# Kernel tuning notes

Hardware: AMD Instinct MI355X
Metric: run time of the kernel (lower is better)

Reference implementation:

```python
import jax, jax.numpy as jnp
import numpy as np

M1 = M2 = M3 = 8  # truncated Hartley modes (min(modes, in_channels) in original)


def dht(x):
    # Discrete Hartley transform via 3D FFT over spatial axes: real - imag
    r = jnp.fft.fftn(x, axes=(2, 3, 4))
    return r.real - r.imag


def _mul(a, w):
    # 'bixyz,ioxyz->boxyz' mode-wise channel mixing
    return jnp.einsum('bixyz,ioxyz->boxyz', a, w)


def setup_inputs() -> dict:
    key = jax.random.key(0)
    ks = jax.random.split(key, 5)
    B, Ci, Co = 2, 64, 64
    S1 = S2 = S3 = 64
    scale = 1.0 / (Ci * Co)
    x = jax.random.normal(ks[0], (B, Ci, S1, S2, S3), dtype=jnp.float32)
    wshape = (Ci, Co, M1, M2, M3)
    w1 = scale * jax.random.uniform(ks[1], wshape, dtype=jnp.float32)
    w2 = scale * jax.random.uniform(ks[2], wshape, dtype=jnp.float32)
    w3 = scale * jax.random.uniform(ks[3], wshape, dtype=jnp.float32)
    w4 = scale * jax.random.uniform(ks[4], wshape, dtype=jnp.float32)
    return {"x": x, "w1": w1, "w2": w2, "w3": w3, "w4": w4}


def reference(x, w1, w2, w3, w4):
    b, ci, s1, s2, s3 = x.shape
    co = w1.shape[1]
    # Hartley transform of x ("cos part") and of fully flipped x ("sin part")
    xh = dht(x)
    xhf = dht(x[:, :, ::-1, ::-1, ::-1])

    out_ht = jnp.zeros((b, co, s1, s2, s3), dtype=x.dtype)
    out_ht = out_ht.at[:, :, :M1, :M2, :M3].set(_mul(xh[:, :, :M1, :M2, :M3], w1))
    out_ht = out_ht.at[:, :, -M1:, :M2, :M3].set(_mul(xh[:, :, -M1:, :M2, :M3], w2))
    out_ht = out_ht.at[:, :, :M1, -M2:, :M3].set(_mul(xh[:, :, :M1, -M2:, :M3], w3))
    out_ht = out_ht.at[:, :, -M1:, -M2:, :M3].set(_mul(xh[:, :, -M1:, -M2:, :M3], w4))
    # original zeroes out_ht[:, :, M1:, M2:, M3:] — already zero here since 2*modes <= size

    # inverse DHT = DHT / (D*M*N)
    x_rec = dht(out_ht) / (s1 * s2 * s3)

    # phase = angle(complex(cos_part, sin_part)) = atan2(sin, cos), only on corner block; 0 elsewhere
    phase_corner = jnp.arctan2(xhf[:, :, :M1, :M2, :M3], xh[:, :, :M1, :M2, :M3])
    cos_phase = jnp.ones((b, ci, s1, s2, s3), dtype=x.dtype)
    cos_phase = cos_phase.at[:, :, :M1, :M2, :M3].set(jnp.cos(phase_corner))
    return x_rec * cos_phase
```

## Files before the change

### kernel.cpp

```cpp
#include <hip/hip_runtime.h>
#include <math.h>

struct cf2 { float x, y; };
struct TW64 { float c[64], s[64]; };
struct CF2T { cf2 v[64]; };

constexpr double PI_D = 3.14159265358979323846264338327950288;

constexpr double tsin(double x){
  double x2 = x*x, r = x, t = x;
  t *= -x2/6.0;   r += t;
  t *= -x2/20.0;  r += t;
  t *= -x2/42.0;  r += t;
  t *= -x2/72.0;  r += t;
  t *= -x2/110.0; r += t;
  t *= -x2/156.0; r += t;
  t *= -x2/210.0; r += t;
  t *= -x2/272.0; r += t;
  return r;
}
constexpr double tcos(double x){
  double x2 = x*x, r = 1.0, t = 1.0;
  t *= -x2/2.0;   r += t;
  t *= -x2/12.0;  r += t;
  t *= -x2/30.0;  r += t;
  t *= -x2/56.0;  r += t;
  t *= -x2/90.0;  r += t;
  t *= -x2/132.0; r += t;
  t *= -x2/182.0; r += t;
  t *= -x2/240.0; r += t;
  return r;
}
constexpr double ang_cos(int j){
  int r = j & 15, q = (j >> 4) & 3;
  double a = PI_D/32.0 * r;
  double cc = tcos(a), ss = tsin(a);
  return q==0 ? cc : q==1 ? -ss : q==2 ? -cc : ss;
}
constexpr double ang_sin(int j){
  int r = j & 15, q = (j >> 4) & 3;
  double a = PI_D/32.0 * r;
  double cc = tcos(a), ss = tsin(a);
  return q==0 ? ss : q==1 ? cc : q==2 ? -ss : -cc;
}
constexpr TW64 make_tw(){
  TW64 t{};
  for (int j=0;j<64;j++){ t.c[j] = (float)ang_cos(j); t.s[j] = (float)ang_sin(j); }
  return t;
}
constexpr CF2T make_twi(){
  CF2T r{};
  for (int j=0;j<64;j++){ r.v[j].x = (float)ang_cos(j); r.v[j].y = (float)ang_sin(j); }
  return r;
}
constexpr CF2T make_pq(){
  CF2T r{};
  for (int j=0;j<64;j++){
    double c = ang_cos(j), s = ang_sin(j);
    r.v[j].x = (float)((c + s) / 262144.0);
    r.v[j].y = (float)((s - c) / 262144.0);
  }
  return r;
}

constexpr TW64 TWct = make_tw();
__constant__ CF2T TWIdev = make_twi();
__constant__ CF2T PQdev  = make_pq();


template<int G>
__device__ __forceinline__ void stageA(const float* __restrict__ row,
                                       float& r0, float& i0, float& r1, float& i1){
  r0=0.f; i0=0.f; r1=0.f; i1=0.f;
  #pragma unroll
  for (int n3=0;n3<64;n3++){
    float xv = row[n3];
    r0 = fmaf(xv,  TWct.c[((2*G  )*n3)&63], r0);
    i0 = fmaf(xv, -TWct.s[((2*G  )*n3)&63], i0);
    r1 = fmaf(xv,  TWct.c[((2*G+1)*n3)&63], r1);
    i1 = fmaf(xv, -TWct.s[((2*G+1)*n3)&63], i1);
  }
}

__global__ __launch_bounds__(256) void k_fwd(const float* __restrict__ x, float2* __restrict__ y2g){
  __shared__ float xt[64*65];
  __shared__ float2 y1[8*66];
  __shared__ cf2 twl[64];
  int bid = blockIdx.x;
  int n1 = bid & 63, ci_b = bid >> 6;
  int t = threadIdx.x;
  if (t < 64) twl[t] = TWIdev.v[t];

  const float4* src = (const float4*)(x + (size_t)(ci_b*64 + n1)*4096);
  #pragma unroll
  for (int j=0;j<4;j++){
    int q = t + j*256;
    float4 v = src[q];
    int n2 = q >> 4, n3 = (q & 15)*4;
    float* d = &xt[n2*65 + n3];
    d[0]=v.x; d[1]=v.y; d[2]=v.z; d[3]=v.w;
  }
  __syncthreads();

  {
    int n2 = t & 63, g = t >> 6;
    const float* row = &xt[n2*65];
    float r0,i0,r1,i1;
    if      (g==0) stageA<0>(row,r0,i0,r1,i1);
    else if (g==1) stageA<1>(row,r0,i0,r1,i1);
    else if (g==2) stageA<2>(row,r0,i0,r1,i1);
    else           stageA<3>(row,r0,i0,r1,i1);
    y1[(2*g  )*66 + n2] = make_float2(r0,i0);
    y1[(2*g+1)*66 + n2] = make_float2(r1,i1);
  }
  __syncthreads();

  {
    int half = t & 1, k3 = (t >> 1) & 7, k2i = t >> 4;
    int k2 = k2i < 8 ? k2i : 48 + k2i;
    int idx = (k2 * (half*32)) & 63;
    const float2* yrow = &y1[k3*66 + half*32];
    float ar = 0.f, ai = 0.f;
    #pragma unroll 8
    for (int i=0;i<32;i++){
      cf2 tw = twl[idx];
      idx = (idx + k2) & 63;
      float2 y = yrow[i];
      ar = fmaf(y.x, tw.x, fmaf(y.y, tw.y, ar));
      ai = fmaf(y.y, tw.x, fmaf(-y.x, tw.y, ai));
    }
    ar += __shfl_xor(ar, 1, 64);
    ai += __shfl_xor(ai, 1, 64);
    if (half == 0){
      y2g[((size_t)(ci_b*64 + n1)*16 + k2i)*8 + k3] = make_float2(ar, ai);
    }
  }
}

template<int K1B>
__device__ __forceinline__ void k2_body(const float2 (*yl)[128], int kk, float* ar, float* ai){
  for (int n1=0;n1<64;n1++){
    float2 y = yl[n1][kk];
    #pragma unroll
    for (int j=0;j<8;j++){
      int k1i = K1B + 2*j;
      int k1 = k1i < 8 ? k1i : 48 + k1i;
      cf2 tw = TWIdev.v[(k1*n1)&63];
      ar[j] = fmaf(y.x, tw.x, fmaf(y.y, tw.y, ar[j]));
      ai[j] = fmaf(y.y, tw.x, fmaf(-y.x, tw.y, ai[j]));
    }
  }
}

__global__ __launch_bounds__(256) void k_fwd_n1(const float2* __restrict__ y2g,
                                                float* __restrict__ xh, float* __restrict__ cp){
  __shared__ float2 yl[64][128];
  int bc = blockIdx.x;
  int t = threadIdx.x;
  const float2* src = y2g + (size_t)bc * 8192;
  #pragma unroll
  for (int j=0;j<32;j++){
    int idx = t + j*256;
    yl[idx>>7][idx&127] = src[idx];
  }
  __syncthreads();
  int kk = t & 127;
  int k2i = kk >> 3, k3 = kk & 7;
  float ar[8], ai[8];
  #pragma unroll
  for (int j=0;j<8;j++){ ar[j]=0.f; ai[j]=0.f; }
  if (t < 128) k2_body<0>(yl, kk, ar, ai);
  else         k2_body<1>(yl, kk, ar, ai);
  int k1base = t >> 7;
  size_t xbase = (size_t)bc * 2048;
  #pragma unroll
  for (int j=0;j<8;j++){
    int k1i = k1base + 2*j;
    float vr = ar[j], vi = ai[j];
    float vxh = vr - vi;
    xh[xbase + k1i*128 + kk] = vxh;
    if (k1i < 8 && k2i < 8){
      int phi = (k1i + k2i + k3) & 63;
      cf2 tw = TWIdev.v[phi];
      float vxhf = vr*(tw.x - tw.y) + vi*(tw.x + tw.y);
      cp[(size_t)bc*512 + k1i*64 + k2i*8 + k3] = cosf(atan2f(vxhf, vxh));
    }
  }
}

__global__ __launch_bounds__(256) void k_mix(const float* __restrict__ xh,
    const float* __restrict__ w1, const float* __restrict__ w2,
    const float* __restrict__ w3, const float* __restrict__ w4,
    float* __restrict__ mh){
  __shared__ float xs[2][64][64];
  __shared__ float wsh[64][64];
  __shared__ float ps[2][128];
  int bid = blockIdx.x;
  int k1l = bid & 7, co = (bid >> 3) & 63, blk = bid >> 9;
  const float* w = (blk==0) ? w1 : (blk==1) ? w2 : (blk==2) ? w3 : w4;
  int k1i = k1l + ((blk & 1) << 3);
  int k2off = (blk & 2) ? 64 : 0;
  int t = threadIdx.x;
  #pragma unroll
  for (int j=0;j<16;j++){
    int idx = t + j*256;
    int ci = idx >> 6, kk = idx & 63;
    wsh[ci][kk] = w[(size_t)(ci*64 + co)*512 + k1l*64 + kk];
  }
  #pragma unroll
  for (int j=0;j<32;j++){
    int idx = t + j*256;
    int b = idx >> 12, ci = (idx >> 6) & 63, kk = idx & 63;
    xs[b][ci][kk] = xh[(size_t)((b*64 + ci)*16 + k1i)*128 + k2off + kk];
  }
  __syncthreads();
  int half = t >> 7, o = t & 127, b = o >> 6, kk = o & 63;
  float acc = 0.f;
  #pragma unroll 8
  for (int i=0;i<32;i++){
    int ci = half*32 + i;
    acc = fmaf(xs[b][ci][kk], wsh[ci][kk], acc);
  }
  ps[half][o] = acc;
  __syncthreads();
  if (t < 128){
    int b2 = t >> 6, kk2 = t & 63;
    mh[(size_t)((b2*64 + co)*16 + k1i)*128 + k2off + kk2] = ps[0][t] + ps[1][t];
  }
}

__global__ __launch_bounds__(256) void k_inv(const float* __restrict__ mh,
                                             const float* __restrict__ cp,
                                             float* __restrict__ out){
  __shared__ float ml[2048];
  __shared__ float2 z1[16][8];
  __shared__ float2 z2[64][8];
  __shared__ cf2 twl[64];
  __shared__ cf2 pql[64];
  int bid = blockIdx.x;
  int n1 = bid & 63, bc = bid >> 6;
  int t = threadIdx.x;
  if (t < 64){ twl[t] = TWIdev.v[t]; pql[t] = PQdev.v[t]; }
  const float* src = mh + (size_t)bc * 2048;
  #pragma unroll
  for (int j=0;j<8;j++) ml[t + j*256] = src[t + j*256];
  __syncthreads();
  if (t < 128){
    float zr = 0.f, zi = 0.f;
    #pragma unroll
    for (int k1i=0;k1i<16;k1i++){
      int k1 = k1i < 8 ? k1i : 48 + k1i;
      cf2 tw = TWIdev.v[(k1*n1)&63];
      float m = ml[k1i*128 + t];
      zr = fmaf(m, tw.x, zr);
      zi = fmaf(m, -tw.y, zi);
    }
    z1[t>>3][t&7] = make_float2(zr, zi);
  }
  __syncthreads();
  #pragma unroll
  for (int jo=0;jo<2;jo++){
    int o = t + jo*256;
    int n2 = o >> 3, k3 = o & 7;
    float zr = 0.f, zi = 0.f;
    #pragma unroll
    for (int k2i=0;k2i<16;k2i++){
      int k2 = k2i < 8 ? k2i : 48 + k2i;
      cf2 tw = twl[(k2*n2)&63];
      float2 z = z1[k2i][k3];
      zr = fmaf(z.x, tw.x, fmaf(z.y, tw.y, zr));
      zi = fmaf(z.y, tw.x, fmaf(-z.x, tw.y, zi));
    }
    z2[n2][k3] = make_float2(zr, zi);
  }
  __syncthreads();
  int n3 = t & 63;
  int n2base = (t >> 6) * 16;
  float p[8], q[8];
  #pragma unroll
  for (int k3=0;k3<8;k3++){
    cf2 pq = pql[(k3*n3)&63];
    p[k3] = pq.x; q[k3] = pq.y;
  }
  float* orow = out + ((size_t)bc*64 + n1)*4096;
  bool corner = (n1 < 8) && (n3 < 8);
  const float* cpr = cp + (size_t)bc*512 + n1*64 + n3;
  #pragma unroll
  for (int j=0;j<16;j++){
    int n2 = n2base + j;
    float v = 0.f;
    #pragma unroll
    for (int k3=0;k3<8;k3++){
      float2 z = z2[n2][k3];
      v = fmaf(z.x, p[k3], fmaf(z.y, q[k3], v));
    }
    if (corner && n2 < 8) v *= cpr[n2*8];
    orow[n2*64 + n3] = v;
  }
}

extern "C" void kernel_launch(void* const* d_in, const int* in_sizes, int n_in,
                              void* d_out, int out_size, void* d_ws, size_t ws_size,
                              hipStream_t stream) {
  (void)in_sizes; (void)n_in; (void)out_size; (void)ws_size;
  const float* x  = (const float*)d_in[0];
  const float* w1 = (const float*)d_in[1];
  const float* w2 = (const float*)d_in[2];
  const float* w3 = (const float*)d_in[3];
  const float* w4 = (const float*)d_in[4];
  float* out = (float*)d_out;
  char* ws = (char*)d_ws;
  float2* y2g = (float2*)ws;
  float*  xh  = (float*)(ws + (8u<<20));
  float*  cp  = (float*)(ws + (9u<<20));
  float*  mh  = (float*)(ws + (9u<<20) + (256u<<10));

  k_fwd   <<<8192, 256, 0, stream>>>(x, y2g);
  k_fwd_n1<<< 128, 256, 0, stream>>>(y2g, xh, cp);
  k_mix   <<<2048, 256, 0, stream>>>(xh, w1, w2, w3, w4, mh);
  k_inv   <<<8192, 256, 0, stream>>>(mh, cp, out);
}
```

Before: 296.7 us.

## Restructure forward DFT stages, add twiddle recurrences and vectorized loads

k_fwd now processes two n1 planes per block, with each thread computing four k3 modes from float4 shared-memory loads. Its k2 stage replaces table lookups with a rotating-phasor recurrence. k_fwd_n1 is re-split from 128 blocks to 2048 blocks (one per bc and k2i) and uses a recurrence with a shuffle reduction, which greatly raises parallelism in that stage. k_mix, k_inv loads and the final k3 sum switch to float4 accesses, and k_inv's k2 sum also uses recurrences. The recurrences trade table reads for sequential FMA dependency and may accumulate small rounding error.

```diff
diff --git a/kernel.cpp b/kernel.cpp
--- a/kernel.cpp
+++ b/kernel.cpp
@@ -69,120 +69,113 @@
 
 
 template<int G>
-__device__ __forceinline__ void stageA(const float* __restrict__ row,
-                                       float& r0, float& i0, float& r1, float& i1){
-  r0=0.f; i0=0.f; r1=0.f; i1=0.f;
-  #pragma unroll
-  for (int n3=0;n3<64;n3++){
-    float xv = row[n3];
-    r0 = fmaf(xv,  TWct.c[((2*G  )*n3)&63], r0);
-    i0 = fmaf(xv, -TWct.s[((2*G  )*n3)&63], i0);
-    r1 = fmaf(xv,  TWct.c[((2*G+1)*n3)&63], r1);
-    i1 = fmaf(xv, -TWct.s[((2*G+1)*n3)&63], i1);
+__device__ __forceinline__ void stageA4(const float* __restrict__ row, float* a){
+  #pragma unroll
+  for (int m=0;m<8;m++) a[m]=0.f;
+  #pragma unroll
+  for (int qd=0;qd<16;qd++){
+    float4 v = ((const float4*)row)[qd];
+    float xv[4] = {v.x, v.y, v.z, v.w};
+    #pragma unroll
+    for (int u=0;u<4;u++){
+      int n3 = qd*4 + u;
+      #pragma unroll
+      for (int m=0;m<4;m++){
+        a[2*m  ] = fmaf(xv[u],  TWct.c[((G+m)*n3)&63], a[2*m  ]);
+        a[2*m+1] = fmaf(xv[u], -TWct.s[((G+m)*n3)&63], a[2*m+1]);
+      }
+    }
   }
 }
 
 __global__ __launch_bounds__(256) void k_fwd(const float* __restrict__ x, float2* __restrict__ y2g){
-  __shared__ float xt[64*65];
-  __shared__ float2 y1[8*66];
+  __shared__ alignas(16) float xt[2][64][72];
+  __shared__ alignas(16) float2 y1[2][8][66];
   __shared__ cf2 twl[64];
   int bid = blockIdx.x;
-  int n1 = bid & 63, ci_b = bid >> 6;
+  int pp = bid & 31, ci_b = bid >> 5;
   int t = threadIdx.x;
   if (t < 64) twl[t] = TWIdev.v[t];
 
-  const float4* src = (const float4*)(x + (size_t)(ci_b*64 + n1)*4096);
-  #pragma unroll
-  for (int j=0;j<4;j++){
+  const float4* src = (const float4*)(x + (size_t)(ci_b*64 + pp*2)*4096);
+  #pragma unroll
+  for (int j=0;j<8;j++){
     int q = t + j*256;
     float4 v = src[q];
-    int n2 = q >> 4, n3 = (q & 15)*4;
-    float* d = &xt[n2*65 + n3];
+    int n1l = q >> 10, r = q & 1023;
+    int n2 = r >> 4, n3q = r & 15;
+    float* d = &xt[n1l][n2][n3q*4];
     d[0]=v.x; d[1]=v.y; d[2]=v.z; d[3]=v.w;
   }
   __syncthreads();
 
   {
-    int n2 = t & 63, g = t >> 6;
-    const float* row = &xt[n2*65];
-    float r0,i0,r1,i1;
-    if      (g==0) stageA<0>(row,r0,i0,r1,i1);
-    else if (g==1) stageA<1>(row,r0,i0,r1,i1);
-    else if (g==2) stageA<2>(row,r0,i0,r1,i1);
-    else           stageA<3>(row,r0,i0,r1,i1);
-    y1[(2*g  )*66 + n2] = make_float2(r0,i0);
-    y1[(2*g+1)*66 + n2] = make_float2(r1,i1);
+    int n2 = t & 63, g = (t>>6)&1, n1l = t>>7;
+    const float* row = &xt[n1l][n2][0];
+    float a[8];
+    if (g==0) stageA4<0>(row, a); else stageA4<4>(row, a);
+    #pragma unroll
+    for (int m=0;m<4;m++) y1[n1l][4*g+m][n2] = make_float2(a[2*m], a[2*m+1]);
   }
   __syncthreads();
 
   {
-    int half = t & 1, k3 = (t >> 1) & 7, k2i = t >> 4;
-    int k2 = k2i < 8 ? k2i : 48 + k2i;
-    int idx = (k2 * (half*32)) & 63;
-    const float2* yrow = &y1[k3*66 + half*32];
-    float ar = 0.f, ai = 0.f;
-    #pragma unroll 8
-    for (int i=0;i<32;i++){
-      cf2 tw = twl[idx];
-      idx = (idx + k2) & 63;
-      float2 y = yrow[i];
-      ar = fmaf(y.x, tw.x, fmaf(y.y, tw.y, ar));
-      ai = fmaf(y.y, tw.x, fmaf(-y.x, tw.y, ai));
-    }
-    ar += __shfl_xor(ar, 1, 64);
-    ai += __shfl_xor(ai, 1, 64);
-    if (half == 0){
-      y2g[((size_t)(ci_b*64 + n1)*16 + k2i)*8 + k3] = make_float2(ar, ai);
-    }
-  }
-}
-
-template<int K1B>
-__device__ __forceinline__ void k2_body(const float2 (*yl)[128], int kk, float* ar, float* ai){
-  for (int n1=0;n1<64;n1++){
-    float2 y = yl[n1][kk];
-    #pragma unroll
-    for (int j=0;j<8;j++){
-      int k1i = K1B + 2*j;
-      int k1 = k1i < 8 ? k1i : 48 + k1i;
-      cf2 tw = TWIdev.v[(k1*n1)&63];
-      ar[j] = fmaf(y.x, tw.x, fmaf(y.y, tw.y, ar[j]));
-      ai[j] = fmaf(y.y, tw.x, fmaf(-y.x, tw.y, ai[j]));
-    }
+    int n1l = t>>7, s = t&127, k2i = s>>3, k3 = s&7;
+    int k2 = k2i<8 ? k2i : 48+k2i;
+    cf2 st = twl[k2];
+    float c = 1.f, sn = 0.f, ar = 0.f, ai = 0.f;
+    const float4* yrow = (const float4*)&y1[n1l][k3][0];
+    #pragma unroll
+    for (int m=0;m<32;m++){
+      float4 v = yrow[m];
+      ar = fmaf(v.x, c, fmaf(v.y, sn, ar));
+      ai = fmaf(v.y, c, fmaf(-v.x, sn, ai));
+      float c2 = fmaf(c, st.x, -(sn*st.y));
+      float s2 = fmaf(sn, st.x,  c*st.y);
+      ar = fmaf(v.z, c2, fmaf(v.w, s2, ar));
+      ai = fmaf(v.w, c2, fmaf(-v.z, s2, ai));
+      c  = fmaf(c2, st.x, -(s2*st.y));
+      sn = fmaf(s2, st.x,  c2*st.y);
+    }
+    y2g[(size_t)(ci_b*64 + pp*2 + n1l)*128 + s] = make_float2(ar, ai);
   }
 }
 
 __global__ __launch_bounds__(256) void k_fwd_n1(const float2* __restrict__ y2g,
                                                 float* __restrict__ xh, float* __restrict__ cp){
-  __shared__ float2 yl[64][128];
-  int bc = blockIdx.x;
+  __shared__ alignas(16) float2 yl[64][8];
+  __shared__ cf2 twl[64];
+  int bc = blockIdx.x >> 4, k2i = blockIdx.x & 15;
   int t = threadIdx.x;
-  const float2* src = y2g + (size_t)bc * 8192;
-  #pragma unroll
-  for (int j=0;j<32;j++){
-    int idx = t + j*256;
-    yl[idx>>7][idx&127] = src[idx];
-  }
-  __syncthreads();
-  int kk = t & 127;
-  int k2i = kk >> 3, k3 = kk & 7;
-  float ar[8], ai[8];
-  #pragma unroll
-  for (int j=0;j<8;j++){ ar[j]=0.f; ai[j]=0.f; }
-  if (t < 128) k2_body<0>(yl, kk, ar, ai);
-  else         k2_body<1>(yl, kk, ar, ai);
-  int k1base = t >> 7;
-  size_t xbase = (size_t)bc * 2048;
-  #pragma unroll
-  for (int j=0;j<8;j++){
-    int k1i = k1base + 2*j;
-    float vr = ar[j], vi = ai[j];
-    float vxh = vr - vi;
-    xh[xbase + k1i*128 + kk] = vxh;
+  if (t < 64) twl[t] = TWIdev.v[t];
+  {
+    int n1 = t >> 2, q = t & 3;
+    const float4* s4 = (const float4*)(y2g + ((size_t)(bc*64 + n1)*128 + k2i*8));
+    ((float4*)&yl[n1][0])[q] = s4[q];
+  }
+  __syncthreads();
+  int half = t&1, k3 = (t>>1)&7, k1i = t>>4;
+  int k1 = k1i<8 ? k1i : 48+k1i;
+  cf2 st = twl[k1];
+  cf2 cs = twl[(k1*half*32)&63];
+  float c = cs.x, sn = cs.y, ar = 0.f, ai = 0.f;
+  #pragma unroll
+  for (int i=0;i<32;i++){
+    float2 y = yl[half*32+i][k3];
+    ar = fmaf(y.x, c, fmaf(y.y, sn, ar));
+    ai = fmaf(y.y, c, fmaf(-y.x, sn, ai));
+    float c2 = fmaf(c, st.x, -(sn*st.y));
+    sn = fmaf(sn, st.x,  c*st.y);
+    c = c2;
+  }
+  ar += __shfl_xor(ar, 1, 64);
+  ai += __shfl_xor(ai, 1, 64);
+  if (half == 0){
+    float vxh = ar - ai;
+    xh[(size_t)(bc*16 + k1i)*128 + k2i*8 + k3] = vxh;
     if (k1i < 8 && k2i < 8){
-      int phi = (k1i + k2i + k3) & 63;
-      cf2 tw = TWIdev.v[phi];
-      float vxhf = vr*(tw.x - tw.y) + vi*(tw.x + tw.y);
+      cf2 tw = twl[(k1i + k2i + k3) & 63];
+      float vxhf = ar*(tw.x - tw.y) + ai*(tw.x + tw.y);
       cp[(size_t)bc*512 + k1i*64 + k2i*8 + k3] = cosf(atan2f(vxhf, vxh));
     }
   }
@@ -192,8 +185,8 @@
     const float* __restrict__ w1, const float* __restrict__ w2,
     const float* __restrict__ w3, const float* __restrict__ w4,
     float* __restrict__ mh){
-  __shared__ float xs[2][64][64];
-  __shared__ float wsh[64][64];
+  __shared__ alignas(16) float xs[2][64][64];
+  __shared__ alignas(16) float wsh[64][64];
   __shared__ float ps[2][128];
   int bid = blockIdx.x;
   int k1l = bid & 7, co = (bid >> 3) & 63, blk = bid >> 9;
@@ -202,16 +195,18 @@
   int k2off = (blk & 2) ? 64 : 0;
   int t = threadIdx.x;
   #pragma unroll
-  for (int j=0;j<16;j++){
-    int idx = t + j*256;
-    int ci = idx >> 6, kk = idx & 63;
-    wsh[ci][kk] = w[(size_t)(ci*64 + co)*512 + k1l*64 + kk];
-  }
-  #pragma unroll
-  for (int j=0;j<32;j++){
-    int idx = t + j*256;
-    int b = idx >> 12, ci = (idx >> 6) & 63, kk = idx & 63;
-    xs[b][ci][kk] = xh[(size_t)((b*64 + ci)*16 + k1i)*128 + k2off + kk];
+  for (int jj=0;jj<4;jj++){
+    int idx = t + jj*256;
+    int ci = idx >> 4, kq = idx & 15;
+    float4 v = *(const float4*)(w + (size_t)(ci*64 + co)*512 + k1l*64 + kq*4);
+    ((float4*)&wsh[ci][0])[kq] = v;
+  }
+  #pragma unroll
+  for (int jj=0;jj<8;jj++){
+    int idx = t + jj*256;
+    int b = idx >> 10, ci = (idx >> 4) & 63, kq = idx & 15;
+    float4 v = *(const float4*)(xh + (size_t)((b*64 + ci)*16 + k1i)*128 + k2off + kq*4);
+    ((float4*)&xs[b][ci][0])[kq] = v;
   }
   __syncthreads();
   int half = t >> 7, o = t & 127, b = o >> 6, kk = o & 63;
@@ -232,18 +227,18 @@
 __global__ __launch_bounds__(256) void k_inv(const float* __restrict__ mh,
                                              const float* __restrict__ cp,
                                              float* __restrict__ out){
-  __shared__ float ml[2048];
-  __shared__ float2 z1[16][8];
-  __shared__ float2 z2[64][8];
+  __shared__ alignas(16) float ml[2048];
+  __shared__ alignas(16) float2 z1[16][8];
+  __shared__ alignas(16) float2 z2[64][8];
   __shared__ cf2 twl[64];
   __shared__ cf2 pql[64];
   int bid = blockIdx.x;
   int n1 = bid & 63, bc = bid >> 6;
   int t = threadIdx.x;
   if (t < 64){ twl[t] = TWIdev.v[t]; pql[t] = PQdev.v[t]; }
-  const float* src = mh + (size_t)bc * 2048;
-  #pragma unroll
-  for (int j=0;j<8;j++) ml[t + j*256] = src[t + j*256];
+  const float4* src = (const float4*)(mh + (size_t)bc * 2048);
+  ((float4*)ml)[t]       = src[t];
+  ((float4*)ml)[t + 256] = src[t + 256];
   __syncthreads();
   if (t < 128){
     float zr = 0.f, zi = 0.f;
@@ -262,14 +257,28 @@
   for (int jo=0;jo<2;jo++){
     int o = t + jo*256;
     int n2 = o >> 3, k3 = o & 7;
+    cf2 st = twl[n2];
     float zr = 0.f, zi = 0.f;
-    #pragma unroll
-    for (int k2i=0;k2i<16;k2i++){
-      int k2 = k2i < 8 ? k2i : 48 + k2i;
-      cf2 tw = twl[(k2*n2)&63];
+    float c = 1.f, sn = 0.f;
+    #pragma unroll
+    for (int k2i=0;k2i<8;k2i++){
       float2 z = z1[k2i][k3];
-      zr = fmaf(z.x, tw.x, fmaf(z.y, tw.y, zr));
-      zi = fmaf(z.y, tw.x, fmaf(-z.x, tw.y, zi));
+      zr = fmaf(z.x, c, fmaf(z.y, sn, zr));
+      zi = fmaf(z.y, c, fmaf(-z.x, sn, zi));
+      float c2 = fmaf(c, st.x, -(sn*st.y));
+      sn = fmaf(sn, st.x, c*st.y);
+      c = c2;
+    }
+    cf2 cs = twl[(56*n2)&63];
+    c = cs.x; sn = cs.y;
+    #pragma unroll
+    for (int k2i=8;k2i<16;k2i++){
+      float2 z = z1[k2i][k3];
+      zr = fmaf(z.x, c, fmaf(z.y, sn, zr));
+      zi = fmaf(z.y, c, fmaf(-z.x, sn, zi));
+      float c2 = fmaf(c, st.x, -(sn*st.y));
+      sn = fmaf(sn, st.x, c*st.y);
+      c = c2;
     }
     z2[n2][k3] = make_float2(zr, zi);
   }
@@ -288,12 +297,17 @@
   #pragma unroll
   for (int j=0;j<16;j++){
     int n2 = n2base + j;
-    float v = 0.f;
-    #pragma unroll
-    for (int k3=0;k3<8;k3++){
-      float2 z = z2[n2][k3];
-      v = fmaf(z.x, p[k3], fmaf(z.y, q[k3], v));
-    }
+    const float4* zr4 = (const float4*)&z2[n2][0];
+    float4 u0 = zr4[0], u1 = zr4[1], u2 = zr4[2], u3 = zr4[3];
+    float v;
+    v = fmaf(u0.x, p[0], u0.y*q[0]);
+    v = fmaf(u0.z, p[1], fmaf(u0.w, q[1], v));
+    v = fmaf(u1.x, p[2], fmaf(u1.y, q[2], v));
+    v = fmaf(u1.z, p[3], fmaf(u1.w, q[3], v));
+    v = fmaf(u2.x, p[4], fmaf(u2.y, q[4], v));
+    v = fmaf(u2.z, p[5], fmaf(u2.w, q[5], v));
+    v = fmaf(u3.x, p[6], fmaf(u3.y, q[6], v));
+    v = fmaf(u3.z, p[7], fmaf(u3.w, q[7], v));
     if (corner && n2 < 8) v *= cpr[n2*8];
     orow[n2*64 + n3] = v;
   }
@@ -315,8 +329,8 @@
   float*  cp  = (float*)(ws + (9u<<20));
   float*  mh  = (float*)(ws + (9u<<20) + (256u<<10));
 
-  k_fwd   <<<8192, 256, 0, stream>>>(x, y2g);
-  k_fwd_n1<<< 128, 256, 0, stream>>>(y2g, xh, cp);
+  k_fwd   <<<4096, 256, 0, stream>>>(x, y2g);
+  k_fwd_n1<<<2048, 256, 0, stream>>>(y2g, xh, cp);
   k_mix   <<<2048, 256, 0, stream>>>(xh, w1, w2, w3, w4, mh);
   k_inv   <<<8192, 256, 0, stream>>>(mh, cp, out);
 }
```

Result: faster. 287.7 us (-3.0%).
